# Optimization experiments

Measured on AMD Instinct MI355X. Metric: run time of the kernel, lower is better.

## Reference

```python
import jax, jax.numpy as jnp
import numpy as np
import math

B, T, C_EMB, H, M, P = 4, 8192, 1024, 16, 64, 8
D = C_EMB // H
L = int(math.log2(T // M)) - 1  # = 6 levels of coarse attention
SCALE_ATTN = True
NEG = -1e30


def setup_inputs() -> dict:
    key = jax.random.key(0)
    ks = jax.random.split(key, 4)
    x = jax.random.normal(ks[0], (B, T, C_EMB), jnp.float32)
    W_attn = jax.random.normal(ks[1], (C_EMB, 3 * C_EMB), jnp.float32) * (1.0 / math.sqrt(C_EMB))
    b_attn = jnp.zeros((3 * C_EMB,), jnp.float32)
    W_proj = jax.random.normal(ks[2], (C_EMB, C_EMB), jnp.float32) * (1.0 / math.sqrt(C_EMB))
    b_proj = jnp.zeros((C_EMB,), jnp.float32)
    return {"x": x, "W_attn": W_attn, "b_attn": b_attn, "W_proj": W_proj, "b_proj": b_proj}


def _shift(t, s):
    # shift blocks forward along axis 1 by s, zero-padding at the front
    pad = jnp.zeros_like(t[:, :s])
    return jnp.concatenate([pad, t[:, :-s]], axis=1)


def _fma_attention(q, k, v):
    # q, k, v: [BH, T, D]; q already scaled by 1/sqrt(D)
    BH = q.shape[0]
    # --- convolute(): avgpool downsampled K, V at each level ---
    Kls, Vls = [k], [v]
    for l in range(L):
        r = (M * 2 ** l) // P  # pool kernel = stride
        Kls.append(k.reshape(BH, T // r, r, D).mean(axis=2))
        Vls.append(v.reshape(BH, T // r, r, D).mean(axis=2))
    # --- stage1: banded QK at every level ---
    As = []
    # fine level 0: causal sliding window of M keys (j in [i-M+1, i])
    nb0 = T // M
    qb = q.reshape(BH, nb0, M, D)
    kb = k.reshape(BH, nb0, M, D)
    s_prev = jnp.einsum('bgqd,bgkd->bgqk', qb, _shift(kb, 1))
    s_self = jnp.einsum('bgqd,bgkd->bgqk', qb, kb)
    r_idx = jnp.arange(M)[:, None]
    c_idx = jnp.arange(M)[None, :]
    g_ok = (jnp.arange(nb0) >= 1)[None, :, None, None]
    s_prev = jnp.where((c_idx > r_idx) & g_ok, s_prev, NEG)
    s_self = jnp.where(c_idx <= r_idx, s_self, NEG)
    As.append(jnp.concatenate([s_prev, s_self], axis=-1).reshape(BH, T, 2 * M))
    # coarse levels l=1..L: query block (width w) attends to the P summaries of
    # each of the two preceding coarse blocks (causal, left-to-right)
    for l in range(1, L + 1):
        w = M * 2 ** (l - 1)
        nb = T // w
        qw = q.reshape(BH, nb, w, D)
        kc = Kls[l].reshape(BH, nb, P, D)
        scores = []
        for s in (2, 1):
            sc = jnp.einsum('bgqd,bgpd->bgqp', qw, _shift(kc, s))
            ok = (jnp.arange(nb) >= s)[None, :, None, None]
            scores.append(jnp.where(ok, sc, NEG))
        As.append(jnp.concatenate(scores, axis=-1).reshape(BH, T, 2 * P))
    # --- fused multi-level softmax (shared max + shared normalizer) ---
    gmax = jnp.max(jnp.stack([a.max(axis=-1) for a in As], axis=-1), axis=-1)  # [BH, T]
    Es = [jnp.exp(a - gmax[..., None]) for a in As]
    scales = [1] + [((M * 2 ** (l - 1)) // P if SCALE_ATTN else 1) for l in range(1, L + 1)]
    denom = sum(float(s) * e.sum(axis=-1) for s, e in zip(scales, Es))[..., None]
    Cs = [float(s) * e / denom for s, e in zip(scales, Es)]
    # --- stage2: banded CV ---
    vb = v.reshape(BH, nb0, M, D)
    C0 = Cs[0].reshape(BH, nb0, M, 2 * M)
    out = (jnp.einsum('bgqk,bgkd->bgqd', C0[..., :M], _shift(vb, 1)) +
           jnp.einsum('bgqk,bgkd->bgqd', C0[..., M:], vb)).reshape(BH, T, D)
    for l in range(1, L + 1):
        w = M * 2 ** (l - 1)
        nb = T // w
        vc = Vls[l].reshape(BH, nb, P, D)
        Cl = Cs[l].reshape(BH, nb, w, 2 * P)
        ol = (jnp.einsum('bgqp,bgpd->bgqd', Cl[..., :P], _shift(vc, 2)) +
              jnp.einsum('bgqp,bgpd->bgqd', Cl[..., P:], _shift(vc, 1)))
        out = out + ol.reshape(BH, T, D)
    return out


def reference(x, W_attn, b_attn, W_proj, b_proj):
    Bx, Tx, Cx = x.shape
    qkv = x @ W_attn + b_attn
    q, k, v = jnp.split(qkv, 3, axis=-1)

    def heads(t):
        return t.reshape(Bx, Tx, H, D).transpose(0, 2, 1, 3).reshape(Bx * H, Tx, D)

    q = heads(q) / math.sqrt(D)
    o = _fma_attention(q, heads(k), heads(v))
    o = o.reshape(Bx, H, Tx, D).transpose(0, 2, 1, 3).reshape(Bx, Tx, Cx)
    return o @ W_proj + b_proj
```

## Files before the change

kernel.cpp:

```cpp
#include <hip/hip_runtime.h>
#include <hip/hip_bf16.h>
#include <stdint.h>


typedef float  f32x4  __attribute__((ext_vector_type(4)));
typedef __bf16 bf16x8 __attribute__((ext_vector_type(8)));
typedef unsigned short ushort8 __attribute__((ext_vector_type(8)));
typedef unsigned short ushort4v __attribute__((ext_vector_type(4)));
typedef unsigned uint4v __attribute__((ext_vector_type(4)));

__device__ __forceinline__ unsigned short f2bf(float f) {
  union { float f; unsigned u; } v; v.f = f;
  unsigned r = v.u + 0x7fffu + ((v.u >> 16) & 1u);
  return (unsigned short)(r >> 16);
}
__device__ __forceinline__ float bf2f(unsigned short s) {
  union { unsigned u; float f; } v; v.u = ((unsigned)s) << 16;
  return v.f;
}
__device__ __forceinline__ bf16x8 ld_bf8(const unsigned short* p) {
  return __builtin_bit_cast(bf16x8, *(const ushort8*)p);
}
__device__ __forceinline__ f32x4 mfma16(bf16x8 a, bf16x8 b, f32x4 c) {
  return __builtin_amdgcn_mfma_f32_16x16x32_bf16(a, b, c, 0, 0, 0);
}
__device__ __forceinline__ f32x4 zero4() {
  f32x4 z; z[0] = 0.f; z[1] = 0.f; z[2] = 0.f; z[3] = 0.f; return z;
}
__device__ __forceinline__ void gload16(const void* g, void* lds) {
  __builtin_amdgcn_global_load_lds(
      (const __attribute__((address_space(1))) void*)(uintptr_t)g,
      (__attribute__((address_space(3))) void*)(unsigned int)(uintptr_t)lds,
      16, 0, 0);
}

#define T_SEQ 8192
#define NPOOL 2016

#define SCHED0() __builtin_amdgcn_sched_barrier(0)
#define VMC(n)                                           \
  do {                                                   \
    SCHED0();                                            \
    asm volatile("s_waitcnt vmcnt(" #n ")" ::: "memory");\
    SCHED0();                                            \
  } while (0)

__global__ __launch_bounds__(256) void castx_k(const float* __restrict__ x,
                                               unsigned short* __restrict__ xb) {
  size_t i = ((size_t)blockIdx.x * 256 + threadIdx.x) * 8;
  float4 a = *(const float4*)(x + i);
  float4 b = *(const float4*)(x + i + 4);
  ushort8 o;
  o[0] = f2bf(a.x); o[1] = f2bf(a.y); o[2] = f2bf(a.z); o[3] = f2bf(a.w);
  o[4] = f2bf(b.x); o[5] = f2bf(b.y); o[6] = f2bf(b.z); o[7] = f2bf(b.w);
  *(ushort8*)(xb + i) = o;
}

__global__ __launch_bounds__(256) void transposeW_k(const float* __restrict__ w,
                                                    unsigned short* __restrict__ wt,
                                                    int R, int C) {
  __shared__ float tile[64 * 65];
  int cc = blockIdx.x, rc = blockIdx.y;
  int tid = threadIdx.x;
#pragma unroll
  for (int p = 0; p < 4; ++p) {
    int ci = p * 256 + tid;
    int r = ci >> 4, q4 = ci & 15;
    float4 v = *(const float4*)(w + (size_t)(rc * 64 + r) * C + cc * 64 + q4 * 4);
    tile[r * 65 + q4 * 4 + 0] = v.x;
    tile[r * 65 + q4 * 4 + 1] = v.y;
    tile[r * 65 + q4 * 4 + 2] = v.z;
    tile[r * 65 + q4 * 4 + 3] = v.w;
  }
  __syncthreads();
#pragma unroll
  for (int p = 0; p < 2; ++p) {
    int orow = p * 32 + (tid >> 3), tg = tid & 7;
    ushort8 ov;
#pragma unroll
    for (int i = 0; i < 8; ++i) ov[i] = f2bf(tile[(tg * 8 + i) * 65 + orow]);
    *(ushort8*)(wt + (size_t)(cc * 64 + orow) * R + rc * 64 + tg * 8) = ov;
  }
}

template<int NTILE_N, int EPI>
__global__ __launch_bounds__(512, 2) void gemm256(
    const unsigned short* __restrict__ A, const unsigned short* __restrict__ Bt,
    const float* __restrict__ bias,
    unsigned short* __restrict__ o0, unsigned short* __restrict__ o1,
    unsigned short* __restrict__ o2, float* __restrict__ fout) {
  extern __shared__ __align__(16) char smem[];
  const int K = 1024;
  const int nwg = 128 * NTILE_N;
  const int q = nwg >> 3;
  const int wg = ((int)blockIdx.x & 7) * q + ((int)blockIdx.x >> 3);
  const int tm = wg & 127, tn = wg >> 7;
  const int tid = threadIdx.x;
  const int wid = tid >> 6, lane = tid & 63;
  const int wm = wid >> 2, wn = wid & 3;
  const int lr = lane & 15, lg = lane >> 4;

  const int srow = tid >> 2;
  const int sseg = (tid & 3) ^ ((tid >> 3) & 3);
  const unsigned short* aSrc = A + (size_t)(tm * 256 + srow) * K + sseg * 8;
  const unsigned short* bSrc = Bt + (size_t)(tn * 256 + srow) * K + sseg * 8;
  const unsigned ldsT = (unsigned)tid * 16;

  const unsigned psel = (unsigned)((lg ^ ((lr >> 1) & 3)) * 16);
  const unsigned aBase = (unsigned)(wm * 8192 + lr * 64) + psel;
  const unsigned bBase = (unsigned)(16384 + wn * 4096 + lr * 64) + psel;

  f32x4 acc[8][4];
#pragma unroll
  for (int i = 0; i < 8; ++i)
#pragma unroll
    for (int j = 0; j < 4; ++j) acc[i][j] = zero4();

  bf16x8 rA0[4], rA1[4], rB0[4], rB1[4];

  auto SB = [&]() {
    SCHED0();
    __builtin_amdgcn_s_barrier();
    SCHED0();
  };
  auto stage2 = [&](int coffShorts, unsigned slotB) {
#pragma unroll
    for (int pass = 0; pass < 2; ++pass) {
      gload16(aSrc + (size_t)pass * 128 * K + coffShorts,
              smem + slotB + pass * 8192 + ldsT);
      gload16(bSrc + (size_t)pass * 128 * K + coffShorts,
              smem + slotB + 16384 + pass * 8192 + ldsT);
    }
  };
  auto rdA = [&](bf16x8 (&dst)[4], unsigned slotB, int ih) {
    const char* p = smem + slotB + aBase + ih * 4096;
#pragma unroll
    for (int ii = 0; ii < 4; ++ii)
      dst[ii] = ld_bf8((const unsigned short*)(p + ii * 1024));
  };
  auto rdB = [&](bf16x8 (&dst)[4], unsigned slotB) {
    const char* p = smem + slotB + bBase;
#pragma unroll
    for (int j = 0; j < 4; ++j)
      dst[j] = ld_bf8((const unsigned short*)(p + j * 1024));
  };
  auto cluster = [&](int rb, bf16x8 (&a)[4], bf16x8 (&b)[4]) {
    __builtin_amdgcn_s_setprio(1);
#pragma unroll
    for (int ii = 0; ii < 4; ++ii)
#pragma unroll
      for (int j = 0; j < 4; ++j)
        acc[rb + ii][j] = mfma16(b[j], a[ii], acc[rb + ii][j]);
    __builtin_amdgcn_s_setprio(0);
  };

  stage2(0, 0u);
  stage2(32, 32768u);
  stage2(64, 65536u);
  stage2(96, 98304u);
  VMC(12);
  SB();
  rdA(rA0, 0u, 0);
  rdB(rB0, 0u);

  for (int t = 0; t < 16; ++t) {
    const unsigned s0  = (unsigned)((2 * t) & 3) * 32768u;
    const unsigned s1  = (unsigned)((2 * t + 1) & 3) * 32768u;
    const unsigned sn0 = (unsigned)((2 * t + 2) & 3) * 32768u;
    rdA(rA1, s0, 1);
    if (t < 15) { VMC(8); } else { VMC(0); }
    SB();
    cluster(0, rA0, rB0);
    if (t < 14) stage2((t + 2) * 64, s0);
    rdA(rA0, s1, 0);
    rdB(rB1, s1);
    SB();
    cluster(4, rA1, rB0);
    rdA(rA1, s1, 1);
    if (t < 14) { VMC(8); } else if (t == 14) { VMC(4); }
    SB();
    cluster(0, rA0, rB1);
    if (t < 14) stage2((t + 2) * 64 + 32, s1);
    if (t < 15) { rdA(rA0, sn0, 0); rdB(rB0, sn0); }
    SB();
    cluster(4, rA1, rB1);
  }

  const int mBase = tm * 256 + wm * 128;
  const int nBase = tn * 256 + wn * 64;
  if (EPI == 0) {
    const int region = nBase >> 10, nn = nBase & 1023, hh = nn >> 6;
    unsigned short* dst = region == 0 ? o0 : (region == 1 ? o1 : o2);
#pragma unroll
    for (int j = 0; j < 4; ++j) {
      const int d0 = (nn & 63) + j * 16 + lg * 4;
      const float4 bv = *(const float4*)(bias + nBase + j * 16 + lg * 4);
#pragma unroll
      for (int i = 0; i < 8; ++i) {
        const int m = mBase + i * 16 + lr;
        const int bb = m >> 13, tq = m & 8191;
        ushort4v pk;
        pk[0] = f2bf(acc[i][j][0] + bv.x);
        pk[1] = f2bf(acc[i][j][1] + bv.y);
        pk[2] = f2bf(acc[i][j][2] + bv.z);
        pk[3] = f2bf(acc[i][j][3] + bv.w);
        *(ushort4v*)(dst + (((size_t)(bb * 16 + hh)) * T_SEQ + tq) * 64 + d0) = pk;
      }
    }
  } else {
#pragma unroll
    for (int j = 0; j < 4; ++j) {
      const int n0 = nBase + j * 16 + lg * 4;
      const float4 bv = *(const float4*)(bias + n0);
#pragma unroll
      for (int i = 0; i < 8; ++i) {
        const int m = mBase + i * 16 + lr;
        float4 ov;
        ov.x = acc[i][j][0] + bv.x;
        ov.y = acc[i][j][1] + bv.y;
        ov.z = acc[i][j][2] + bv.z;
        ov.w = acc[i][j][3] + bv.w;
        *(float4*)(fout + (size_t)m * 1024 + n0) = ov;
      }
    }
  }
}

__global__ __launch_bounds__(256) void transposeV_k(const unsigned short* __restrict__ v,
                                                    unsigned short* __restrict__ vt) {
  __shared__ float tile[64 * 65];
  int tc = blockIdx.x, bh = blockIdx.y;
  int tid = threadIdx.x;
#pragma unroll
  for (int p = 0; p < 2; ++p) {
    int r = p * 32 + (tid >> 3), cg = tid & 7;
    ushort8 u = *(const ushort8*)(v + ((size_t)bh * T_SEQ + (size_t)tc * 64 + r) * 64 + cg * 8);
#pragma unroll
    for (int i = 0; i < 8; ++i) tile[r * 65 + cg * 8 + i] = bf2f(u[i]);
  }
  __syncthreads();
#pragma unroll
  for (int p = 0; p < 2; ++p) {
    int dd = p * 32 + (tid >> 3), tg = tid & 7;
    ushort8 ov;
#pragma unroll
    for (int i = 0; i < 8; ++i) ov[i] = f2bf(tile[(tg * 8 + i) * 65 + dd]);
    *(ushort8*)(vt + ((size_t)bh * 64 + dd) * T_SEQ + (size_t)tc * 64 + tg * 8) = ov;
  }
}

__global__ __launch_bounds__(256) void poolK_k(const unsigned short* __restrict__ kin,
                                               unsigned short* __restrict__ kpool) {
  __shared__ float buf[64 * 65];
  int chunk = blockIdx.x, bh = blockIdx.y;
  int tid = threadIdx.x;
  int cg = tid & 7, orow = tid >> 3;
  float s[8];
#pragma unroll
  for (int i = 0; i < 8; ++i) s[i] = 0.f;
  const unsigned short* base =
      kin + ((size_t)bh * T_SEQ + chunk * 256 + orow * 8) * 64 + cg * 8;
#pragma unroll
  for (int rr = 0; rr < 8; ++rr) {
    ushort8 v = *(const ushort8*)(base + (size_t)rr * 64);
#pragma unroll
    for (int i = 0; i < 8; ++i) s[i] += bf2f(v[i]);
  }
  unsigned short* kp = kpool + (size_t)bh * NPOOL * 64;
  {
    ushort8 ov;
#pragma unroll
    for (int i = 0; i < 8; ++i) {
      s[i] *= 0.125f;
      ov[i] = f2bf(s[i]);
      buf[orow * 65 + cg * 8 + i] = s[i];
    }
    *(ushort8*)(kp + ((size_t)(chunk * 32 + orow)) * 64 + cg * 8) = ov;
  }
  __syncthreads();
  int srcR = 0, dstR = 32;
#pragma unroll
  for (int lvl = 2; lvl <= 6; ++lvl) {
    int rows = 32 >> (lvl - 1);
    int off = 2048 - (2048 >> (lvl - 1));
    if (orow < rows) {
      ushort8 ov;
      float tv[8];
#pragma unroll
      for (int i = 0; i < 8; ++i) {
        tv[i] = 0.5f * (buf[(srcR + 2 * orow) * 65 + cg * 8 + i] +
                        buf[(srcR + 2 * orow + 1) * 65 + cg * 8 + i]);
        ov[i] = f2bf(tv[i]);
      }
      *(ushort8*)(kp + ((size_t)(off + chunk * rows + orow)) * 64 + cg * 8) = ov;
#pragma unroll
      for (int i = 0; i < 8; ++i) buf[(dstR + orow) * 65 + cg * 8 + i] = tv[i];
    }
    __syncthreads();
    srcR = dstR;
    dstR += rows;
  }
}

__global__ __launch_bounds__(256) void poolV_k(const unsigned short* __restrict__ vt,
                                               unsigned short* __restrict__ vtpool) {
  __shared__ float buf[1024 + 512 + 256 + 128 + 64];
  int d = blockIdx.x, bh = blockIdx.y;
  int tid = threadIdx.x;
  const unsigned short* src = vt + ((size_t)bh * 64 + d) * T_SEQ;
  unsigned short* dst = vtpool + ((size_t)bh * 64 + d) * NPOOL;
#pragma unroll
  for (int p = 0; p < 4; ++p) {
    int oi = p * 256 + tid;
    ushort8 v = *(const ushort8*)(src + (size_t)oi * 8);
    float s = 0.f;
#pragma unroll
    for (int i = 0; i < 8; ++i) s += bf2f(v[i]);
    s *= 0.125f;
    dst[oi] = f2bf(s);
    buf[oi] = s;
  }
  __syncthreads();
  float* b1 = buf; float* b2 = buf + 1024;
#pragma unroll
  for (int p = 0; p < 2; ++p) {
    int oi = p * 256 + tid;
    float s = 0.5f * (b1[2 * oi] + b1[2 * oi + 1]);
    dst[1024 + oi] = f2bf(s);
    b2[oi] = s;
  }
  __syncthreads();
  float* b3 = b2 + 512;
  {
    float s = 0.5f * (b2[2 * tid] + b2[2 * tid + 1]);
    dst[1536 + tid] = f2bf(s);
    b3[tid] = s;
  }
  __syncthreads();
  float* b4 = b3 + 256;
  if (tid < 128) {
    float s = 0.5f * (b3[2 * tid] + b3[2 * tid + 1]);
    dst[1792 + tid] = f2bf(s);
    b4[tid] = s;
  }
  __syncthreads();
  float* b5 = b4 + 128;
  if (tid < 64) {
    float s = 0.5f * (b4[2 * tid] + b4[2 * tid + 1]);
    dst[1920 + tid] = f2bf(s);
    b5[tid] = s;
  }
  __syncthreads();
  if (tid < 32) {
    float s = 0.5f * (b5[2 * tid] + b5[2 * tid + 1]);
    dst[1984 + tid] = f2bf(s);
  }
}

__global__ __launch_bounds__(256, 4) void attn_k(const unsigned short* __restrict__ q,
                                                 const unsigned short* __restrict__ k,
                                                 const unsigned short* __restrict__ kpool,
                                                 const unsigned short* __restrict__ vt,
                                                 const unsigned short* __restrict__ vtpool,
                                                 unsigned short* __restrict__ o) {
  const int bidx = (int)blockIdx.x;
  const int g = (bidx & 7) * 16 + (bidx >> 3);
  const int bh = blockIdx.y;
  const int tid = threadIdx.x;
  const int w = tid >> 6, l = tid & 63;
  const int lr = l & 15, lg = l >> 4;
  __shared__ unsigned short KV[224 * 64];

  const size_t qoff = ((size_t)bh * T_SEQ + (size_t)g * 64 + w * 16 + lr) * 64 + lg * 8;
  bf16x8 aq0 = ld_bf8(q + qoff);
  bf16x8 aq1 = ld_bf8(q + qoff + 32);
  SCHED0();

  const int krow = tid >> 3;
  const int kseg = tid & 7;
#pragma unroll
  for (int p = 0; p < 7; ++p) {
    const int row = p * 32 + krow;
    const unsigned short* src;
    if (row < 128) {
      int t0 = (g - 1) * 64 + row;
      if (t0 < 0) t0 = 0;
      src = k + ((size_t)bh * T_SEQ + t0) * 64;
    } else {
      const int pr = row - 128;
      const int lvl0 = pr >> 4;
      const int off = 2048 - (2048 >> lvl0);
      const int gl = g >> lvl0;
      int st = (gl - 2) * 8 + (pr & 15);
      if (st < 0) st = 0;
      src = kpool + ((size_t)bh * NPOOL + off + st) * 64;
    }
    gload16(src + (kseg ^ (row & 7)) * 8,
            ((char*)KV) + p * 4096 + (unsigned)tid * 16);
  }
  VMC(0);
  __builtin_amdgcn_s_barrier();
  SCHED0();

  f32x4 S[14];
#pragma unroll
  for (int ct = 0; ct < 14; ++ct) S[ct] = zero4();
#pragma unroll
  for (int ct = 0; ct < 14; ++ct) {
    const int row = ct * 16 + lr;
    const unsigned short* kr = KV + row * 64;
    const int sw = row & 7;
    S[ct] = mfma16(ld_bf8(kr + (lg ^ sw) * 8), aq0, S[ct]);
    S[ct] = mfma16(ld_bf8(kr + ((lg + 4) ^ sw) * 8), aq1, S[ct]);
  }
  SCHED0();
  __builtin_amdgcn_s_barrier();
  SCHED0();

  const int vr = tid >> 2;
  const int vg = tid & 3;
  const int vswz = vg ^ ((vr >> 1) & 3);
#pragma unroll
  for (int s = 0; s < 7; ++s) {
    const int colsh = s * 32 + vswz * 8;
    const unsigned short* src;
    if (colsh < 128) {
      int t0 = (g - 1) * 64 + colsh;
      if (t0 < 0) t0 = 0;
      src = vt + ((size_t)bh * 64 + vr) * T_SEQ + t0;
    } else {
      const int c = colsh - 128;
      const int lvl = c >> 4;
      const int off = 2048 - (2048 >> lvl);
      const int gl = g >> lvl;
      int start = (gl - 2) * 8 + (c & 15);
      if (start < 0) start = 0;
      src = vtpool + ((size_t)bh * 64 + vr) * NPOOL + off + start;
    }
    gload16(src, ((char*)KV) + s * 4096 + (unsigned)tid * 16);
  }
  SCHED0();

  const float NEGF = -1e30f;
  const int qq = w * 16 + lr;
#pragma unroll
  for (int ct = 0; ct < 14; ++ct) {
#pragma unroll
    for (int e = 0; e < 4; ++e) {
      float s = S[ct][e] * 0.125f;
      bool valid;
      if (ct < 8) {
        int kk = ct * 16 + lg * 4 + e;
        valid = (kk > qq) && (kk <= qq + 64) && ((g >= 1) || (kk >= 64));
      } else {
        int lvl = ct - 7;
        int gl = g >> (lvl - 1);
        valid = gl >= ((lg < 2) ? 2 : 1);
      }
      S[ct][e] = valid ? s : NEGF;
    }
  }
  float mx = S[0][0];
#pragma unroll
  for (int ct = 0; ct < 14; ++ct)
#pragma unroll
    for (int e = 0; e < 4; ++e) mx = fmaxf(mx, S[ct][e]);
  mx = fmaxf(mx, __shfl_xor(mx, 16));
  mx = fmaxf(mx, __shfl_xor(mx, 32));
  float sum = 0.f;
#pragma unroll
  for (int ct = 0; ct < 14; ++ct) {
    const float sc = (ct < 8) ? 1.0f : (float)(8 << (ct - 8));
#pragma unroll
    for (int e = 0; e < 4; ++e) {
      float ev = sc * __expf(S[ct][e] - mx);
      S[ct][e] = ev;
      sum += ev;
    }
  }
  sum += __shfl_xor(sum, 16);
  sum += __shfl_xor(sum, 32);
  const float invd = 1.0f / sum;

  unsigned pw[14][2];
#pragma unroll
  for (int ct = 0; ct < 14; ++ct) {
    float p0 = S[ct][0] * invd, p1 = S[ct][1] * invd;
    float p2 = S[ct][2] * invd, p3 = S[ct][3] * invd;
    asm("v_cvt_pk_bf16_f32 %0, %1, %2" : "=v"(pw[ct][0]) : "v"(p0), "v"(p1));
    asm("v_cvt_pk_bf16_f32 %0, %1, %2" : "=v"(pw[ct][1]) : "v"(p2), "v"(p3));
  }

  VMC(0);
  __syncthreads();

  const int src0 = lr + ((lg & 1) << 5);
  const int src1 = src0 + 16;
  const bool odd = (lg & 2) != 0;
  f32x4 O[4];
#pragma unroll
  for (int c2 = 0; c2 < 4; ++c2) O[c2] = zero4();
#pragma unroll
  for (int kc = 0; kc < 7; ++kc) {
    unsigned we0 = __shfl((int)pw[2 * kc][0], src0);
    unsigned we1 = __shfl((int)pw[2 * kc][1], src0);
    unsigned we2 = __shfl((int)pw[2 * kc][0], src1);
    unsigned we3 = __shfl((int)pw[2 * kc][1], src1);
    unsigned wo0 = __shfl((int)pw[2 * kc + 1][0], src0);
    unsigned wo1 = __shfl((int)pw[2 * kc + 1][1], src0);
    unsigned wo2 = __shfl((int)pw[2 * kc + 1][0], src1);
    unsigned wo3 = __shfl((int)pw[2 * kc + 1][1], src1);
    uint4v fw;
    fw[0] = odd ? wo0 : we0;
    fw[1] = odd ? wo1 : we1;
    fw[2] = odd ? wo2 : we2;
    fw[3] = odd ? wo3 : we3;
    bf16x8 paf = __builtin_bit_cast(bf16x8, fw);
#pragma unroll
    for (int c2 = 0; c2 < 4; ++c2) {
      const int row = c2 * 16 + lr;
      bf16x8 vb = ld_bf8(&KV[kc * 2048 + row * 32 + ((lg ^ ((lr >> 1) & 3)) * 8)]);
      O[c2] = mfma16(paf, vb, O[c2]);
    }
  }
  const int bb = bh >> 4, hh = bh & 15;
#pragma unroll
  for (int c2 = 0; c2 < 4; ++c2) {
    int d = c2 * 16 + lr;
#pragma unroll
    for (int e = 0; e < 4; ++e) {
      int t = g * 64 + w * 16 + lg * 4 + e;
      o[((size_t)bb * T_SEQ + t) * 1024 + hh * 64 + d] = f2bf(O[c2][e]);
    }
  }
}

extern "C" void kernel_launch(void* const* d_in, const int* in_sizes, int n_in,
                              void* d_out, int out_size, void* d_ws, size_t ws_size,
                              hipStream_t stream) {
  const float* x  = (const float*)d_in[0];
  const float* Wa = (const float*)d_in[1];
  const float* ba = (const float*)d_in[2];
  const float* Wp = (const float*)d_in[3];
  const float* bp = (const float*)d_in[4];
  float* out = (float*)d_out;
  char* ws = (char*)d_ws;
  const size_t MB = 1024 * 1024;

  unsigned short* xb  = (unsigned short*)(ws);
  unsigned short* qb  = (unsigned short*)(ws + 64 * MB);
  unsigned short* kb  = (unsigned short*)(ws + 128 * MB);
  unsigned short* vb  = (unsigned short*)(ws + 192 * MB);
  unsigned short* vt  = (unsigned short*)(ws + 256 * MB);
  unsigned short* wat = (unsigned short*)(ws + 320 * MB);
  unsigned short* wpt = (unsigned short*)(ws + 326 * MB);
  unsigned short* kpool  = xb;
  unsigned short* vtpool = (unsigned short*)(ws + 32 * MB);

  hipFuncSetAttribute((const void*)gemm256<12, 0>,
                      hipFuncAttributeMaxDynamicSharedMemorySize, 131072);
  hipFuncSetAttribute((const void*)gemm256<4, 1>,
                      hipFuncAttributeMaxDynamicSharedMemorySize, 131072);

  castx_k<<<16384, 256, 0, stream>>>(x, xb);
  transposeW_k<<<dim3(48, 16), 256, 0, stream>>>(Wa, wat, 1024, 3072);
  transposeW_k<<<dim3(16, 16), 256, 0, stream>>>(Wp, wpt, 1024, 1024);
  gemm256<12, 0><<<1536, 512, 131072, stream>>>(xb, wat, ba, qb, kb, vb, nullptr);
  transposeV_k<<<dim3(128, 64), 256, 0, stream>>>(vb, vt);
  poolK_k<<<dim3(32, 64), 256, 0, stream>>>(kb, kpool);
  poolV_k<<<dim3(64, 64), 256, 0, stream>>>(vt, vtpool);
  attn_k<<<dim3(128, 64), 256, 0, stream>>>(qb, kb, kpool, vt, vtpool, vb);
  gemm256<4, 1><<<512, 512, 131072, stream>>>(vb, wpt, bp, nullptr, nullptr, nullptr, out);
}
```

Before: 497.5 us.

## Fuse V transpose with V pooling and prefetch V tiles alongside K in attention

Merges the V transpose and the multi-level V pooling into one kernel, so vt no longer has to be re-read from global memory and one launch is removed. In the attention kernel, V gets its own shared buffer, and its loads are issued before the QK MFMAs, with a partial vmcnt wait that covers only the K loads. This overlaps the V fetch with the score computation. The cost is doubled LDS per block (about 56KB) and the removal of the min-blocks hint in launch_bounds, which may reduce occupancy.

```diff
diff --git a/kernel.cpp b/kernel.cpp
--- a/kernel.cpp
+++ b/kernel.cpp
@@ -226,26 +226,87 @@
   }
 }
 
-__global__ __launch_bounds__(256) void transposeV_k(const unsigned short* __restrict__ v,
-                                                    unsigned short* __restrict__ vt) {
+__global__ __launch_bounds__(256) void vproc_k(const unsigned short* __restrict__ vb,
+                                               unsigned short* __restrict__ vt,
+                                               unsigned short* __restrict__ vtpool) {
   __shared__ float tile[64 * 65];
-  int tc = blockIdx.x, bh = blockIdx.y;
-  int tid = threadIdx.x;
-#pragma unroll
-  for (int p = 0; p < 2; ++p) {
-    int r = p * 32 + (tid >> 3), cg = tid & 7;
-    ushort8 u = *(const ushort8*)(v + ((size_t)bh * T_SEQ + (size_t)tc * 64 + r) * 64 + cg * 8);
-#pragma unroll
-    for (int i = 0; i < 8; ++i) tile[r * 65 + cg * 8 + i] = bf2f(u[i]);
+  __shared__ float pbuf[64 * 33];
+  const int chunk = blockIdx.x;
+  const int bh = blockIdx.y;
+  const int tid = threadIdx.x;
+
+#pragma unroll
+  for (int s = 0; s < 4; ++s) {
+    const int tbase = chunk * 256 + s * 64;
+#pragma unroll
+    for (int p = 0; p < 2; ++p) {
+      int r = p * 32 + (tid >> 3), cg = tid & 7;
+      ushort8 u = *(const ushort8*)(vb + ((size_t)bh * T_SEQ + tbase + r) * 64 + cg * 8);
+#pragma unroll
+      for (int i = 0; i < 8; ++i) tile[r * 65 + cg * 8 + i] = bf2f(u[i]);
+    }
+    __syncthreads();
+#pragma unroll
+    for (int p = 0; p < 2; ++p) {
+      int dd = p * 32 + (tid >> 3), tg = tid & 7;
+      ushort8 ov;
+      float sum = 0.f;
+#pragma unroll
+      for (int i = 0; i < 8; ++i) {
+        float v = tile[(tg * 8 + i) * 65 + dd];
+        ov[i] = f2bf(v);
+        sum += v;
+      }
+      *(ushort8*)(vt + ((size_t)bh * 64 + dd) * T_SEQ + tbase + tg * 8) = ov;
+      pbuf[dd * 33 + s * 8 + tg] = sum * 0.125f;
+    }
+    __syncthreads();
+  }
+
+  unsigned short* vp = vtpool + ((size_t)bh * 64) * NPOOL;
+  {
+    const int d = tid >> 2, qq = tid & 3;
+    ushort8 ov;
+#pragma unroll
+    for (int i = 0; i < 8; ++i) ov[i] = f2bf(pbuf[d * 33 + qq * 8 + i]);
+    *(ushort8*)(vp + (size_t)d * NPOOL + chunk * 32 + qq * 8) = ov;
+  }
+  {
+    const int d = tid >> 2, qq = tid & 3;
+    ushort4v ov;
+#pragma unroll
+    for (int i = 0; i < 4; ++i) {
+      const int j = qq * 4 + i;
+      float v = 0.5f * (pbuf[d * 33 + 2 * j] + pbuf[d * 33 + 2 * j + 1]);
+      tile[d * 17 + j] = v;
+      ov[i] = f2bf(v);
+    }
+    *(ushort4v*)(vp + (size_t)d * NPOOL + 1024 + chunk * 16 + qq * 4) = ov;
   }
   __syncthreads();
-#pragma unroll
-  for (int p = 0; p < 2; ++p) {
-    int dd = p * 32 + (tid >> 3), tg = tid & 7;
-    ushort8 ov;
-#pragma unroll
-    for (int i = 0; i < 8; ++i) ov[i] = f2bf(tile[(tg * 8 + i) * 65 + dd]);
-    *(ushort8*)(vt + ((size_t)bh * 64 + dd) * T_SEQ + (size_t)tc * 64 + tg * 8) = ov;
+  if (tid < 64) {
+    const int d = tid;
+    float l3[8], l4[4], l5[2];
+    ushort8 o3;
+#pragma unroll
+    for (int j = 0; j < 8; ++j) {
+      l3[j] = 0.5f * (tile[d * 17 + 2 * j] + tile[d * 17 + 2 * j + 1]);
+      o3[j] = f2bf(l3[j]);
+    }
+    *(ushort8*)(vp + (size_t)d * NPOOL + 1536 + chunk * 8) = o3;
+    ushort4v o4;
+#pragma unroll
+    for (int j = 0; j < 4; ++j) {
+      l4[j] = 0.5f * (l3[2 * j] + l3[2 * j + 1]);
+      o4[j] = f2bf(l4[j]);
+    }
+    *(ushort4v*)(vp + (size_t)d * NPOOL + 1792 + chunk * 4) = o4;
+#pragma unroll
+    for (int j = 0; j < 2; ++j) {
+      l5[j] = 0.5f * (l4[2 * j] + l4[2 * j + 1]);
+      vp[(size_t)d * NPOOL + 1920 + chunk * 2 + j] = f2bf(l5[j]);
+    }
+    vp[(size_t)d * NPOOL + 1984 + chunk] = f2bf(0.5f * (l5[0] + l5[1]));
   }
 }
 
@@ -302,67 +363,12 @@
   }
 }
 
-__global__ __launch_bounds__(256) void poolV_k(const unsigned short* __restrict__ vt,
-                                               unsigned short* __restrict__ vtpool) {
-  __shared__ float buf[1024 + 512 + 256 + 128 + 64];
-  int d = blockIdx.x, bh = blockIdx.y;
-  int tid = threadIdx.x;
-  const unsigned short* src = vt + ((size_t)bh * 64 + d) * T_SEQ;
-  unsigned short* dst = vtpool + ((size_t)bh * 64 + d) * NPOOL;
-#pragma unroll
-  for (int p = 0; p < 4; ++p) {
-    int oi = p * 256 + tid;
-    ushort8 v = *(const ushort8*)(src + (size_t)oi * 8);
-    float s = 0.f;
-#pragma unroll
-    for (int i = 0; i < 8; ++i) s += bf2f(v[i]);
-    s *= 0.125f;
-    dst[oi] = f2bf(s);
-    buf[oi] = s;
-  }
-  __syncthreads();
-  float* b1 = buf; float* b2 = buf + 1024;
-#pragma unroll
-  for (int p = 0; p < 2; ++p) {
-    int oi = p * 256 + tid;
-    float s = 0.5f * (b1[2 * oi] + b1[2 * oi + 1]);
-    dst[1024 + oi] = f2bf(s);
-    b2[oi] = s;
-  }
-  __syncthreads();
-  float* b3 = b2 + 512;
-  {
-    float s = 0.5f * (b2[2 * tid] + b2[2 * tid + 1]);
-    dst[1536 + tid] = f2bf(s);
-    b3[tid] = s;
-  }
-  __syncthreads();
-  float* b4 = b3 + 256;
-  if (tid < 128) {
-    float s = 0.5f * (b3[2 * tid] + b3[2 * tid + 1]);
-    dst[1792 + tid] = f2bf(s);
-    b4[tid] = s;
-  }
-  __syncthreads();
-  float* b5 = b4 + 128;
-  if (tid < 64) {
-    float s = 0.5f * (b4[2 * tid] + b4[2 * tid + 1]);
-    dst[1920 + tid] = f2bf(s);
-    b5[tid] = s;
-  }
-  __syncthreads();
-  if (tid < 32) {
-    float s = 0.5f * (b5[2 * tid] + b5[2 * tid + 1]);
-    dst[1984 + tid] = f2bf(s);
-  }
-}
-
-__global__ __launch_bounds__(256, 4) void attn_k(const unsigned short* __restrict__ q,
-                                                 const unsigned short* __restrict__ k,
-                                                 const unsigned short* __restrict__ kpool,
-                                                 const unsigned short* __restrict__ vt,
-                                                 const unsigned short* __restrict__ vtpool,
-                                                 unsigned short* __restrict__ o) {
+__global__ __launch_bounds__(256) void attn_k(const unsigned short* __restrict__ q,
+                                              const unsigned short* __restrict__ k,
+                                              const unsigned short* __restrict__ kpool,
+                                              const unsigned short* __restrict__ vt,
+                                              const unsigned short* __restrict__ vtpool,
+                                              unsigned short* __restrict__ o) {
   const int bidx = (int)blockIdx.x;
   const int g = (bidx & 7) * 16 + (bidx >> 3);
   const int bh = blockIdx.y;
@@ -370,6 +376,7 @@
   const int w = tid >> 6, l = tid & 63;
   const int lr = l & 15, lg = l >> 4;
   __shared__ unsigned short KV[224 * 64];
+  __shared__ unsigned short Vl[224 * 64];
 
   const size_t qoff = ((size_t)bh * T_SEQ + (size_t)g * 64 + w * 16 + lr) * 64 + lg * 8;
   bf16x8 aq0 = ld_bf8(q + qoff);
@@ -398,23 +405,6 @@
     gload16(src + (kseg ^ (row & 7)) * 8,
             ((char*)KV) + p * 4096 + (unsigned)tid * 16);
   }
-  VMC(0);
-  __builtin_amdgcn_s_barrier();
-  SCHED0();
-
-  f32x4 S[14];
-#pragma unroll
-  for (int ct = 0; ct < 14; ++ct) S[ct] = zero4();
-#pragma unroll
-  for (int ct = 0; ct < 14; ++ct) {
-    const int row = ct * 16 + lr;
-    const unsigned short* kr = KV + row * 64;
-    const int sw = row & 7;
-    S[ct] = mfma16(ld_bf8(kr + (lg ^ sw) * 8), aq0, S[ct]);
-    S[ct] = mfma16(ld_bf8(kr + ((lg + 4) ^ sw) * 8), aq1, S[ct]);
-  }
-  SCHED0();
-  __builtin_amdgcn_s_barrier();
   SCHED0();
 
   const int vr = tid >> 2;
@@ -437,7 +427,24 @@
       if (start < 0) start = 0;
       src = vtpool + ((size_t)bh * 64 + vr) * NPOOL + off + start;
     }
-    gload16(src, ((char*)KV) + s * 4096 + (unsigned)tid * 16);
+    gload16(src, ((char*)Vl) + s * 4096 + (unsigned)tid * 16);
+  }
+  SCHED0();
+  asm volatile("s_waitcnt vmcnt(7)" ::: "memory");
+  SCHED0();
+  __builtin_amdgcn_s_barrier();
+  SCHED0();
+
+  f32x4 S[14];
+#pragma unroll
+  for (int ct = 0; ct < 14; ++ct) S[ct] = zero4();
+#pragma unroll
+  for (int ct = 0; ct < 14; ++ct) {
+    const int row = ct * 16 + lr;
+    const unsigned short* kr = KV + row * 64;
+    const int sw = row & 7;
+    S[ct] = mfma16(ld_bf8(kr + (lg ^ sw) * 8), aq0, S[ct]);
+    S[ct] = mfma16(ld_bf8(kr + ((lg + 4) ^ sw) * 8), aq1, S[ct]);
   }
   SCHED0();
 
@@ -519,7 +526,7 @@
 #pragma unroll
     for (int c2 = 0; c2 < 4; ++c2) {
       const int row = c2 * 16 + lr;
-      bf16x8 vb = ld_bf8(&KV[kc * 2048 + row * 32 + ((lg ^ ((lr >> 1) & 3)) * 8)]);
+      bf16x8 vb = ld_bf8(&Vl[kc * 2048 + row * 32 + ((lg ^ ((lr >> 1) & 3)) * 8)]);
       O[c2] = mfma16(paf, vb, O[c2]);
     }
   }
@@ -566,9 +573,8 @@
   transposeW_k<<<dim3(48, 16), 256, 0, stream>>>(Wa, wat, 1024, 3072);
   transposeW_k<<<dim3(16, 16), 256, 0, stream>>>(Wp, wpt, 1024, 1024);
   gemm256<12, 0><<<1536, 512, 131072, stream>>>(xb, wat, ba, qb, kb, vb, nullptr);
-  transposeV_k<<<dim3(128, 64), 256, 0, stream>>>(vb, vt);
+  vproc_k<<<dim3(32, 64), 256, 0, stream>>>(vb, vt, vtpool);
   poolK_k<<<dim3(32, 64), 256, 0, stream>>>(kb, kpool);
-  poolV_k<<<dim3(64, 64), 256, 0, stream>>>(vt, vtpool);
   attn_k<<<dim3(128, 64), 256, 0, stream>>>(qb, kb, kpool, vt, vtpool, vb);
   gemm256<4, 1><<<512, 512, 131072, stream>>>(vb, wpt, bp, nullptr, nullptr, nullptr, out);
 }
```

Result: slower. 516.9 us (+3.9%).
